# Kernel tuning notes

Hardware: AMD Instinct MI355X
Metric: run time of the kernel (lower is better)

## Reference

```python
import jax, jax.numpy as jnp
import numpy as np

B, T, D, E, H = 4, 2048, 1024, 4, 8
EPS = 1e-5


def _uniform(k, shape, bound):
    return jax.random.uniform(k, shape, jnp.float32, -bound, bound)


def setup_inputs() -> dict:
    key = jax.random.key(0)
    ks = jax.random.split(key, 12)
    wb = np.sqrt(6.0 / D) / np.sqrt(6.0)  # kaiming_uniform(a=sqrt5) bound ~ 1/sqrt(D)... keep simple
    wb = 1.0 / np.sqrt(D)
    return {
        "x": jax.random.normal(ks[0], (B, T, D), jnp.float32),
        "router_prob": jax.random.uniform(ks[1], (B, T, E), jnp.float32),
        "norm_w": jnp.ones((D,), jnp.float32),
        "norm_b": jnp.zeros((D,), jnp.float32),
        "q_w": _uniform(ks[2], (D, D), wb),
        "q_b": _uniform(ks[3], (D,), wb),
        "k_w": _uniform(ks[4], (D, D), wb),
        "k_b": _uniform(ks[5], (D,), wb),
        "v_w": _uniform(ks[6], (D, D), wb),
        "v_b": _uniform(ks[7], (D,), wb),
        "o_w": _uniform(ks[8], (D, D), wb),
        "o_b": _uniform(ks[9], (D,), wb),
    }


def _layernorm(x, w, b):
    mu = jnp.mean(x, axis=-1, keepdims=True)
    var = jnp.mean(jnp.square(x - mu), axis=-1, keepdims=True)
    return (x - mu) * jax.lax.rsqrt(var + EPS) * w + b


def reference(x, router_prob, norm_w, norm_b, q_w, q_b, k_w, k_b, v_w, v_b, o_w, o_b):
    e_cnt = router_prob.shape[2]
    b, t, d = x.shape
    n = t // e_cnt
    h = H
    scale = d ** (-0.5)  # note: original uses model_dim**-0.5, not head_dim

    qs, ks_, vs = [], [], []
    for e in range(e_cnt):
        xe = x[:, e * n:(e + 1) * n, :]
        xn = _layernorm(xe, norm_w, norm_b)
        m = d // (2 ** e)
        xm = xn[..., :m]  # [b, n, m] matryoshka slice
        # F.linear(xm, W[:, :m], bias): out = xm @ W[:, :m]^T + b -> [b, n, d]
        qs.append(jnp.einsum('bnm,dm->bnd', xm, q_w[:, :m]) + q_b)
        ks_.append(jnp.einsum('bnm,dm->bnd', xm, k_w[:, :m]) + k_b)
        vs.append(jnp.einsum('bnm,dm->bnd', xm, v_w[:, :m]) + v_b)
    q = jnp.concatenate(qs, axis=1)
    k = jnp.concatenate(ks_, axis=1)
    v = jnp.concatenate(vs, axis=1)

    dh = d // h
    q = q.reshape(b, t, h, dh).transpose(0, 2, 1, 3)  # b h t dh
    k = k.reshape(b, t, h, dh).transpose(0, 2, 1, 3)
    v = v.reshape(b, t, h, dh).transpose(0, 2, 1, 3)

    attn = jnp.einsum('bhqd,bhkd->bhqk', q, k) * scale
    attn = jax.nn.softmax(attn, axis=-1)  # dropout = identity in eval
    attn_out = jnp.einsum('bhqk,bhkd->bhqd', attn, v)
    attn_out = attn_out.transpose(0, 2, 1, 3).reshape(b, t, d)

    outs = []
    for e in range(e_cnt):
        sl = slice(e * n, (e + 1) * n)
        m = d // (2 ** e)
        xm = attn_out[:, sl, :m]
        out = jnp.einsum('bnm,om->bno', xm, o_w[:m, :m]) + o_b[:m]  # [b, n, m]
        pad = d - m
        if pad:
            out = jnp.pad(out, ((0, 0), (0, 0), (0, pad)))
        outs.append(out + x[:, sl, :])
    return jnp.concatenate(outs, axis=1)
```

## Files before the change

### kernel.cpp

```cpp
#include <hip/hip_runtime.h>
#include <hip/hip_bf16.h>

#define DEV static __device__ __forceinline__

typedef __attribute__((ext_vector_type(4))) float f32x4;
typedef __attribute__((ext_vector_type(8))) short s16x8;
typedef __attribute__((ext_vector_type(4))) unsigned int u32x4;

constexpr int Bn = 4, Tn = 2048, Dn = 1024, Hn = 8, DH = 128;
constexpr float EPSF = 1e-5f;
constexpr float QSCALE = 0.0450842200277801f;

DEV unsigned short f2bf(float f) {
    unsigned int u = __float_as_uint(f);
    u += 0x7FFF + ((u >> 16) & 1);
    return (unsigned short)(u >> 16);
}

DEV f32x4 mfma16(s16x8 a, s16x8 b, f32x4 c) {
    return __builtin_amdgcn_mfma_f32_16x16x32_bf16(a, b, c, 0, 0, 0);
}

DEV float ex2(float x) {
    float r;
    asm("v_exp_f32 %0, %1" : "=v"(r) : "v"(x));
    return r;
}

DEV unsigned int cvtpk(float lo, float hi) {
    unsigned int r;
    asm("v_cvt_pk_bf16_f32 %0, %1, %2" : "=v"(r) : "v"(lo), "v"(hi));
    return r;
}

typedef __attribute__((address_space(1))) const unsigned int GU32;
typedef __attribute__((address_space(3))) unsigned int LU32;
DEV void gload16(const void* g, void* l) {
    __builtin_amdgcn_global_load_lds((GU32*)g, (LU32*)l, 16, 0, 0);
}

__global__ __launch_bounds__(256) void cvtln_kernel(const float* __restrict__ x,
                                                    const float* __restrict__ w,
                                                    const float* __restrict__ b,
                                                    const float* __restrict__ qw,
                                                    const float* __restrict__ kw,
                                                    const float* __restrict__ vw,
                                                    const float* __restrict__ ow,
                                                    unsigned short* __restrict__ xn,
                                                    unsigned short* __restrict__ wb) {
    int bid = blockIdx.x;
    int tid = threadIdx.x;
    if (bid >= 8192) {
        int base = (bid - 8192) * 1024 + tid * 4;
        #pragma unroll
        for (int j = 0; j < 4; j++) {
            int idx = base + j;
            int sel = idx >> 20;
            int off = idx & (Dn * Dn - 1);
            const float* src = sel == 0 ? qw : sel == 1 ? kw : sel == 2 ? vw : ow;
            wb[idx] = f2bf(src[off]);
        }
        return;
    }
    int tok = bid;
    const float* xp = x + (size_t)tok * Dn;
    float4 v = ((const float4*)xp)[tid];
    float s = v.x + v.y + v.z + v.w;
    float q = v.x * v.x + v.y * v.y + v.z * v.z + v.w * v.w;
    for (int off = 32; off; off >>= 1) {
        s += __shfl_xor(s, off);
        q += __shfl_xor(q, off);
    }
    __shared__ float red[8];
    __shared__ float stats[2];
    int wid = tid >> 6, lane = tid & 63;
    if (lane == 0) { red[wid] = s; red[4 + wid] = q; }
    __syncthreads();
    if (tid == 0) {
        float ts = red[0] + red[1] + red[2] + red[3];
        float tq = red[4] + red[5] + red[6] + red[7];
        float mu = ts / Dn;
        float var = tq / Dn - mu * mu;
        stats[0] = mu;
        stats[1] = rsqrtf(var + EPSF);
    }
    __syncthreads();
    float mu = stats[0], rs = stats[1];
    int c = tid * 4;
    ushort4 o;
    o.x = f2bf((v.x - mu) * rs * w[c + 0] + b[c + 0]);
    o.y = f2bf((v.y - mu) * rs * w[c + 1] + b[c + 1]);
    o.z = f2bf((v.z - mu) * rs * w[c + 2] + b[c + 2]);
    o.w = f2bf((v.w - mu) * rs * w[c + 3] + b[c + 3]);
    ((ushort4*)(xn + (size_t)tok * Dn))[tid] = o;
}

__global__ __launch_bounds__(256) void qkv_gemm(const unsigned short* __restrict__ xn,
                                                const unsigned short* __restrict__ wmat,
                                                const float* __restrict__ qb_,
                                                const float* __restrict__ kb_,
                                                const float* __restrict__ vb_,
                                                unsigned short* __restrict__ outq,
                                                unsigned short* __restrict__ outk,
                                                unsigned short* __restrict__ vt) {
    int rowbase = blockIdx.x * 128;
    int colbase = blockIdx.y * 128;
    int matid = blockIdx.z;
    const unsigned short* W = wmat + (size_t)matid * Dn * Dn;
    const float* bias = matid == 0 ? qb_ : matid == 1 ? kb_ : vb_;
    float oscale = matid == 0 ? QSCALE : 1.0f;
    int e = (rowbase & (Tn - 1)) >> 9;
    int m = Dn >> e;
    int nt = m >> 5;

    __shared__ alignas(16) unsigned short At[3][128 * 32];
    __shared__ alignas(16) unsigned short Bt[3][128 * 32];

    int tid = threadIdx.x;
    int lane = tid & 63, wv = tid >> 6;
    int wr = (wv >> 1) * 64, wc = (wv & 1) * 64;
    int fr = lane & 15, fg = lane >> 4;
    int srow = tid >> 2, scol = (tid & 3) * 8;
    const unsigned short* ga0 = xn + (size_t)(rowbase + srow) * Dn + scol;
    const unsigned short* ga1 = xn + (size_t)(rowbase + 64 + srow) * Dn + scol;
    const unsigned short* gb0 = W + (size_t)(colbase + srow) * Dn + scol;
    const unsigned short* gb1 = W + (size_t)(colbase + 64 + srow) * Dn + scol;

    f32x4 acc[4][4] = {};

    auto STAGE = [&](int tt, int buf) {
        int kk = tt * 32;
        gload16(ga0 + kk, &At[buf][tid * 8]);
        gload16(ga1 + kk, &At[buf][2048 + tid * 8]);
        gload16(gb0 + kk, &Bt[buf][tid * 8]);
        gload16(gb1 + kk, &Bt[buf][2048 + tid * 8]);
    };

    STAGE(0, 0);
    if (nt > 1) STAGE(1, 1);

    int cur = 0, nxt2 = 2;
    for (int t = 0; t < nt; t++) {
        if (t + 1 < nt) { asm volatile("s_waitcnt vmcnt(4)" ::: "memory"); }
        else            { asm volatile("s_waitcnt vmcnt(0)" ::: "memory"); }
        __builtin_amdgcn_s_barrier();
        if (t + 2 < nt) STAGE(t + 2, nxt2);
        s16x8 a[4], b[4];
        #pragma unroll
        for (int i = 0; i < 4; i++) a[i] = *(const s16x8*)&At[cur][(wr + i * 16 + fr) * 32 + fg * 8];
        #pragma unroll
        for (int j = 0; j < 4; j++) b[j] = *(const s16x8*)&Bt[cur][(wc + j * 16 + fr) * 32 + fg * 8];
        #pragma unroll
        for (int i = 0; i < 4; i++)
            #pragma unroll
            for (int j = 0; j < 4; j++) acc[i][j] = mfma16(a[i], b[j], acc[i][j]);
        cur = cur == 2 ? 0 : cur + 1;
        nxt2 = nxt2 == 2 ? 0 : nxt2 + 1;
    }

    if (matid == 2) {
        #pragma unroll
        for (int i = 0; i < 4; i++)
            #pragma unroll
            for (int j = 0; j < 4; j++) {
                int col = colbase + wc + j * 16 + fr;
                float bv = bias[col];
                int row0 = rowbase + wr + i * 16 + fg * 4;
                int bb = row0 >> 11, tl = row0 & (Tn - 1);
                int w32 = tl & 31;
                int tlp = (tl & ~31) | (((w32 >> 2) & 3) * 8 + ((w32 >> 4) & 1) * 4);
                size_t base = (((size_t)bb * Hn + (col >> 7)) * DH + (col & (DH - 1))) * Tn + tlp;
                ushort4 o;
                o.x = f2bf(acc[i][j][0] + bv);
                o.y = f2bf(acc[i][j][1] + bv);
                o.z = f2bf(acc[i][j][2] + bv);
                o.w = f2bf(acc[i][j][3] + bv);
                *(ushort4*)&vt[base] = o;
            }
    } else {
        unsigned short* out = matid == 0 ? outq : outk;
        #pragma unroll
        for (int i = 0; i < 4; i++)
            #pragma unroll
            for (int j = 0; j < 4; j++) {
                int col = colbase + wc + j * 16 + fr;
                float bv = bias[col];
                #pragma unroll
                for (int r = 0; r < 4; r++) {
                    int row = rowbase + wr + i * 16 + fg * 4 + r;
                    out[(size_t)row * Dn + col] = f2bf((acc[i][j][r] + bv) * oscale);
                }
            }
    }
}

__global__ __launch_bounds__(512, 1) void attn_kernel(const unsigned short* __restrict__ Q,
                                                      const unsigned short* __restrict__ K,
                                                      const unsigned short* __restrict__ VT,
                                                      unsigned short* __restrict__ AO) {
    int f = blockIdx.x;
    int qi = f >> 5;
    int bh = f & 31;
    int b = bh >> 3, h = bh & 7;
    int qbase = qi * 256;
    int tid = threadIdx.x;
    int wv = tid >> 6, lane = tid & 63;
    int fr = lane & 15, fg = lane >> 4;

    __shared__ alignas(16) unsigned short Kt[2][128 * 128];
    __shared__ alignas(16) unsigned short Vt[2][128 * 128];

    s16x8 bq[2][4];
    #pragma unroll
    for (int hh = 0; hh < 2; hh++) {
        const size_t qr = ((size_t)b * Tn + qbase + wv * 32 + hh * 16 + fr) * Dn + h * DH;
        #pragma unroll
        for (int c = 0; c < 4; c++) bq[hh][c] = *(const s16x8*)&Q[qr + c * 32 + fg * 8];
    }

    const s16x8 ones = {(short)0x3F80, (short)0x3F80, (short)0x3F80, (short)0x3F80,
                        (short)0x3F80, (short)0x3F80, (short)0x3F80, (short)0x3F80};

    f32x4 acc[2][9] = {};
    float m_run[2] = {-1e30f, -1e30f};

    const unsigned short* Kbase = K + (size_t)b * Tn * Dn + h * DH;
    const unsigned short* Vbase = VT + ((size_t)b * Hn + h) * DH * Tn;

    int s_row_lo = tid >> 4, s_chk = tid & 15;

    auto STAGE = [&](int t, int buf) {
        int kb = t * 128;
        #pragma unroll
        for (int p = 0; p < 4; p++) {
            int row = p * 32 + s_row_lo;
            int chunk = s_chk ^ (row & 7);
            gload16(Kbase + (size_t)(kb + row) * Dn + chunk * 8,
                    &Kt[buf][p * 4096 + tid * 8]);
        }
        #pragma unroll
        for (int p = 0; p < 4; p++) {
            int row = p * 32 + s_row_lo;
            int chunk = s_chk ^ (row & 15);
            gload16(Vbase + (size_t)row * Tn + kb + chunk * 8,
                    &Vt[buf][p * 4096 + tid * 8]);
        }
    };

    STAGE(0, 0);
    __syncthreads();

    constexpr int NT = Tn / 128;
    for (int t = 0; t < NT; t++) {
        int cur = t & 1;
        if (t < NT - 1) STAGE(t + 1, cur ^ 1);

        const unsigned short* KtC = &Kt[cur][0];
        const unsigned short* VtC = &Vt[cur][0];

        f32x4 s[2][8] = {};
        __builtin_amdgcn_s_setprio(1);
        #pragma unroll
        for (int c = 0; c < 4; c++) {
            #pragma unroll
            for (int kt = 0; kt < 8; kt++) {
                s16x8 ak = *(const s16x8*)&KtC[(kt * 16 + fr) * 128 +
                                               (((c * 4 + fg) ^ (fr & 7)) * 8)];
                s[0][kt] = mfma16(ak, bq[0][c], s[0][kt]);
                s[1][kt] = mfma16(ak, bq[1][c], s[1][kt]);
            }
        }
        __builtin_amdgcn_s_setprio(0);

        float mx[2];
        #pragma unroll
        for (int hh = 0; hh < 2; hh++) {
            float v = s[hh][0][0];
            #pragma unroll
            for (int kt = 0; kt < 8; kt++)
                #pragma unroll
                for (int r = 0; r < 4; r++) v = fmaxf(v, s[hh][kt][r]);
            v = fmaxf(v, __shfl_xor(v, 16));
            v = fmaxf(v, __shfl_xor(v, 32));
            mx[hh] = v;
        }

        if (!__all(mx[0] - m_run[0] <= 8.0f && mx[1] - m_run[1] <= 8.0f)) {
            #pragma unroll
            for (int hh = 0; hh < 2; hh++) {
                float mnew = fmaxf(m_run[hh], mx[hh]);
                float fsc = ex2(m_run[hh] - mnew);
                float fw[4];
                #pragma unroll
                for (int r = 0; r < 4; r++) fw[r] = __shfl(fsc, fg * 4 + r);
                #pragma unroll
                for (int n = 0; n < 9; n++)
                    #pragma unroll
                    for (int r = 0; r < 4; r++) acc[hh][n][r] *= fw[r];
                m_run[hh] = mnew;
            }
        }

        s16x8 pa[2][4];
        #pragma unroll
        for (int hh = 0; hh < 2; hh++) {
            #pragma unroll
            for (int ks = 0; ks < 4; ks++) {
                float p0 = ex2(s[hh][ks * 2 + 0][0] - m_run[hh]);
                float p1 = ex2(s[hh][ks * 2 + 0][1] - m_run[hh]);
                float p2 = ex2(s[hh][ks * 2 + 0][2] - m_run[hh]);
                float p3 = ex2(s[hh][ks * 2 + 0][3] - m_run[hh]);
                float p4 = ex2(s[hh][ks * 2 + 1][0] - m_run[hh]);
                float p5 = ex2(s[hh][ks * 2 + 1][1] - m_run[hh]);
                float p6 = ex2(s[hh][ks * 2 + 1][2] - m_run[hh]);
                float p7 = ex2(s[hh][ks * 2 + 1][3] - m_run[hh]);
                u32x4 pw;
                pw.x = cvtpk(p0, p1);
                pw.y = cvtpk(p2, p3);
                pw.z = cvtpk(p4, p5);
                pw.w = cvtpk(p6, p7);
                pa[hh][ks] = __builtin_bit_cast(s16x8, pw);
            }
        }

        __builtin_amdgcn_s_setprio(1);
        #pragma unroll
        for (int ks = 0; ks < 4; ks++) {
            #pragma unroll
            for (int n = 0; n < 8; n++) {
                int row = n * 16 + fr;
                s16x8 bv = *(const s16x8*)&VtC[row * 128 +
                                               (((ks * 4 + fg) ^ (row & 15)) * 8)];
                acc[0][n] = mfma16(pa[0][ks], bv, acc[0][n]);
                acc[1][n] = mfma16(pa[1][ks], bv, acc[1][n]);
            }
            acc[0][8] = mfma16(pa[0][ks], ones, acc[0][8]);
            acc[1][8] = mfma16(pa[1][ks], ones, acc[1][8]);
        }
        __builtin_amdgcn_s_setprio(0);
        __syncthreads();
    }

    #pragma unroll
    for (int hh = 0; hh < 2; hh++) {
        float rl[4];
        #pragma unroll
        for (int r = 0; r < 4; r++) rl[r] = 1.0f / acc[hh][8][r];
        size_t orow0 = ((size_t)b * Tn + qbase + wv * 32 + hh * 16) * Dn + h * DH;
        for (int n = 0; n < 8; n++)
            for (int r = 0; r < 4; r++) {
                float v = acc[hh][n][r] * rl[r];
                AO[orow0 + (size_t)(fg * 4 + r) * Dn + n * 16 + fr] = f2bf(v);
            }
    }
}

__global__ __launch_bounds__(256) void oproj_gemm(const unsigned short* __restrict__ A,
                                                  const unsigned short* __restrict__ W,
                                                  const float* __restrict__ bias,
                                                  const float* __restrict__ x,
                                                  float* __restrict__ out) {
    int rowbase = blockIdx.x * 128;
    int colbase = blockIdx.y * 128;
    int e = (rowbase & (Tn - 1)) >> 9;
    int m = Dn >> e;
    int tid = threadIdx.x;

    if (colbase >= m) {
        #pragma unroll
        for (int i = 0; i < 16; i++) {
            int idx = i * 256 + tid;
            int r = idx >> 5, c4 = (idx & 31) * 4;
            size_t g = (size_t)(rowbase + r) * Dn + colbase + c4;
            *(float4*)&out[g] = *(const float4*)&x[g];
        }
        return;
    }

    __shared__ alignas(16) unsigned short At[3][128 * 32];
    __shared__ alignas(16) unsigned short Bt[3][128 * 32];
    int lane = tid & 63, wv = tid >> 6;
    int wr = (wv >> 1) * 64, wc = (wv & 1) * 64;
    int fr = lane & 15, fg = lane >> 4;
    int srow = tid >> 2, scol = (tid & 3) * 8;
    const unsigned short* ga0 = A + (size_t)(rowbase + srow) * Dn + scol;
    const unsigned short* ga1 = A + (size_t)(rowbase + 64 + srow) * Dn + scol;
    const unsigned short* gb0 = W + (size_t)(colbase + srow) * Dn + scol;
    const unsigned short* gb1 = W + (size_t)(colbase + 64 + srow) * Dn + scol;
    int nt = m >> 5;

    f32x4 acc[4][4] = {};

    auto STAGE = [&](int tt, int buf) {
        int kk = tt * 32;
        gload16(ga0 + kk, &At[buf][tid * 8]);
        gload16(ga1 + kk, &At[buf][2048 + tid * 8]);
        gload16(gb0 + kk, &Bt[buf][tid * 8]);
        gload16(gb1 + kk, &Bt[buf][2048 + tid * 8]);
    };

    STAGE(0, 0);
    if (nt > 1) STAGE(1, 1);

    int cur = 0, nxt2 = 2;
    for (int t = 0; t < nt; t++) {
        if (t + 1 < nt) { asm volatile("s_waitcnt vmcnt(4)" ::: "memory"); }
        else            { asm volatile("s_waitcnt vmcnt(0)" ::: "memory"); }
        __builtin_amdgcn_s_barrier();
        if (t + 2 < nt) STAGE(t + 2, nxt2);
        s16x8 a[4], b[4];
        #pragma unroll
        for (int i = 0; i < 4; i++) a[i] = *(const s16x8*)&At[cur][(wr + i * 16 + fr) * 32 + fg * 8];
        #pragma unroll
        for (int j = 0; j < 4; j++) b[j] = *(const s16x8*)&Bt[cur][(wc + j * 16 + fr) * 32 + fg * 8];
        #pragma unroll
        for (int i = 0; i < 4; i++)
            #pragma unroll
            for (int j = 0; j < 4; j++) acc[i][j] = mfma16(a[i], b[j], acc[i][j]);
        cur = cur == 2 ? 0 : cur + 1;
        nxt2 = nxt2 == 2 ? 0 : nxt2 + 1;
    }

    #pragma unroll
    for (int i = 0; i < 4; i++)
        #pragma unroll
        for (int j = 0; j < 4; j++) {
            int col = colbase + wc + j * 16 + fr;
            float bv = bias[col];
            #pragma unroll
            for (int r = 0; r < 4; r++) {
                int row = rowbase + wr + i * 16 + fg * 4 + r;
                size_t g = (size_t)row * Dn + col;
                out[g] = acc[i][j][r] + bv + x[g];
            }
        }
}

extern "C" void kernel_launch(void* const* d_in, const int* in_sizes, int n_in,
                              void* d_out, int out_size, void* d_ws, size_t ws_size,
                              hipStream_t stream) {
    const float* x   = (const float*)d_in[0];
    const float* nw  = (const float*)d_in[2];
    const float* nb  = (const float*)d_in[3];
    const float* qw  = (const float*)d_in[4];
    const float* qb_ = (const float*)d_in[5];
    const float* kw  = (const float*)d_in[6];
    const float* kb_ = (const float*)d_in[7];
    const float* vw  = (const float*)d_in[8];
    const float* vb_ = (const float*)d_in[9];
    const float* ow  = (const float*)d_in[10];
    const float* ob_ = (const float*)d_in[11];
    float* out = (float*)d_out;

    unsigned short* ws = (unsigned short*)d_ws;
    const size_t NTOK = (size_t)Bn * Tn;
    unsigned short* xn = ws;
    unsigned short* qd = xn + NTOK * Dn;
    unsigned short* kd = qd + NTOK * Dn;
    unsigned short* vt = kd + NTOK * Dn;
    unsigned short* ao = vt + NTOK * Dn;
    unsigned short* wb = ao + NTOK * Dn;

    hipLaunchKernelGGL(cvtln_kernel, dim3(12288), dim3(256), 0, stream,
                       x, nw, nb, qw, kw, vw, ow, xn, wb);
    hipLaunchKernelGGL(qkv_gemm, dim3(64, 8, 3), dim3(256), 0, stream,
                       xn, wb, qb_, kb_, vb_, qd, kd, vt);
    hipLaunchKernelGGL(attn_kernel, dim3(256), dim3(512), 0, stream, qd, kd, vt, ao);
    hipLaunchKernelGGL(oproj_gemm, dim3(64, 8), dim3(256), 0, stream,
                       ao, wb + (size_t)3 * Dn * Dn, ob_, x, out);
}
```

Baseline: 185.3 us.

## Shrink attention blocks and load V fragments directly from global memory

The attention kernel now uses 256-thread blocks covering 128 queries each, with twice as many blocks and two blocks per CU. The KV tile shrinks from 128 to 64 keys. V is no longer staged in LDS; each lane reads its MFMA B-fragments straight from the transposed V in global memory, and only K stays double-buffered in LDS. This is meant to cut LDS use and raise occupancy, at the cost of uncoalesced, L2-dependent V loads and twice as many loop iterations with barriers.

Measured after the change: 256.8 us. +38.6%, slower.

```diff
diff --git a/kernel.cpp b/kernel.cpp
--- a/kernel.cpp
+++ b/kernel.cpp
@@ -194,7 +194,7 @@
     }
 }
 
-__global__ __launch_bounds__(512, 1) void attn_kernel(const unsigned short* __restrict__ Q,
+__global__ __launch_bounds__(256, 2) void attn_kernel(const unsigned short* __restrict__ Q,
                                                       const unsigned short* __restrict__ K,
                                                       const unsigned short* __restrict__ VT,
                                                       unsigned short* __restrict__ AO) {
@@ -202,13 +202,12 @@
     int qi = f >> 5;
     int bh = f & 31;
     int b = bh >> 3, h = bh & 7;
-    int qbase = qi * 256;
+    int qbase = qi * 128;
     int tid = threadIdx.x;
     int wv = tid >> 6, lane = tid & 63;
     int fr = lane & 15, fg = lane >> 4;
 
-    __shared__ alignas(16) unsigned short Kt[2][128 * 128];
-    __shared__ alignas(16) unsigned short Vt[2][128 * 128];
+    __shared__ alignas(16) unsigned short Kt[2][64 * 128];
 
     s16x8 bq[2][4];
     #pragma unroll
@@ -226,44 +225,38 @@
 
     const unsigned short* Kbase = K + (size_t)b * Tn * Dn + h * DH;
     const unsigned short* Vbase = VT + ((size_t)b * Hn + h) * DH * Tn;
-
-    int s_row_lo = tid >> 4, s_chk = tid & 15;
+    const unsigned short* Vlane = Vbase + (size_t)fr * Tn + fg * 8;
+
+    int k_row_lo = tid >> 4, k_chk = tid & 15;
 
     auto STAGE = [&](int t, int buf) {
-        int kb = t * 128;
+        int kb = t * 64;
         #pragma unroll
         for (int p = 0; p < 4; p++) {
-            int row = p * 32 + s_row_lo;
-            int chunk = s_chk ^ (row & 7);
+            int row = p * 16 + k_row_lo;
+            int chunk = k_chk ^ (row & 7);
             gload16(Kbase + (size_t)(kb + row) * Dn + chunk * 8,
-                    &Kt[buf][p * 4096 + tid * 8]);
-        }
-        #pragma unroll
-        for (int p = 0; p < 4; p++) {
-            int row = p * 32 + s_row_lo;
-            int chunk = s_chk ^ (row & 15);
-            gload16(Vbase + (size_t)row * Tn + kb + chunk * 8,
-                    &Vt[buf][p * 4096 + tid * 8]);
+                    &Kt[buf][p * 2048 + tid * 8]);
         }
     };
 
     STAGE(0, 0);
     __syncthreads();
 
-    constexpr int NT = Tn / 128;
+    constexpr int NT = Tn / 64;
     for (int t = 0; t < NT; t++) {
         int cur = t & 1;
         if (t < NT - 1) STAGE(t + 1, cur ^ 1);
+        int kb = t * 64;
 
         const unsigned short* KtC = &Kt[cur][0];
-        const unsigned short* VtC = &Vt[cur][0];
-
-        f32x4 s[2][8] = {};
+
+        f32x4 s[2][4] = {};
         __builtin_amdgcn_s_setprio(1);
         #pragma unroll
         for (int c = 0; c < 4; c++) {
             #pragma unroll
-            for (int kt = 0; kt < 8; kt++) {
+            for (int kt = 0; kt < 4; kt++) {
                 s16x8 ak = *(const s16x8*)&KtC[(kt * 16 + fr) * 128 +
                                                (((c * 4 + fg) ^ (fr & 7)) * 8)];
                 s[0][kt] = mfma16(ak, bq[0][c], s[0][kt]);
@@ -272,12 +265,19 @@
         }
         __builtin_amdgcn_s_setprio(0);
 
+        s16x8 bv[2][8];
+        #pragma unroll
+        for (int ks = 0; ks < 2; ks++)
+            #pragma unroll
+            for (int n = 0; n < 8; n++)
+                bv[ks][n] = *(const s16x8*)(Vlane + (size_t)(n * 16) * Tn + kb + ks * 32);
+
         float mx[2];
         #pragma unroll
         for (int hh = 0; hh < 2; hh++) {
             float v = s[hh][0][0];
             #pragma unroll
-            for (int kt = 0; kt < 8; kt++)
+            for (int kt = 0; kt < 4; kt++)
                 #pragma unroll
                 for (int r = 0; r < 4; r++) v = fmaxf(v, s[hh][kt][r]);
             v = fmaxf(v, __shfl_xor(v, 16));
@@ -301,38 +301,32 @@
             }
         }
 
-        s16x8 pa[2][4];
+        s16x8 pa[2][2];
         #pragma unroll
         for (int hh = 0; hh < 2; hh++) {
-            #pragma unroll
-            for (int ks = 0; ks < 4; ks++) {
-                float p0 = ex2(s[hh][ks * 2 + 0][0] - m_run[hh]);
-                float p1 = ex2(s[hh][ks * 2 + 0][1] - m_run[hh]);
-                float p2 = ex2(s[hh][ks * 2 + 0][2] - m_run[hh]);
-                float p3 = ex2(s[hh][ks * 2 + 0][3] - m_run[hh]);
-                float p4 = ex2(s[hh][ks * 2 + 1][0] - m_run[hh]);
-                float p5 = ex2(s[hh][ks * 2 + 1][1] - m_run[hh]);
-                float p6 = ex2(s[hh][ks * 2 + 1][2] - m_run[hh]);
-                float p7 = ex2(s[hh][ks * 2 + 1][3] - m_run[hh]);
+            float p[16];
+            #pragma unroll
+            for (int kt = 0; kt < 4; kt++)
+                #pragma unroll
+                for (int r = 0; r < 4; r++) p[kt * 4 + r] = ex2(s[hh][kt][r] - m_run[hh]);
+            #pragma unroll
+            for (int ks = 0; ks < 2; ks++) {
                 u32x4 pw;
-                pw.x = cvtpk(p0, p1);
-                pw.y = cvtpk(p2, p3);
-                pw.z = cvtpk(p4, p5);
-                pw.w = cvtpk(p6, p7);
+                pw.x = cvtpk(p[ks * 8 + 0], p[ks * 8 + 1]);
+                pw.y = cvtpk(p[ks * 8 + 2], p[ks * 8 + 3]);
+                pw.z = cvtpk(p[ks * 8 + 4], p[ks * 8 + 5]);
+                pw.w = cvtpk(p[ks * 8 + 6], p[ks * 8 + 7]);
                 pa[hh][ks] = __builtin_bit_cast(s16x8, pw);
             }
         }
 
         __builtin_amdgcn_s_setprio(1);
         #pragma unroll
-        for (int ks = 0; ks < 4; ks++) {
+        for (int ks = 0; ks < 2; ks++) {
             #pragma unroll
             for (int n = 0; n < 8; n++) {
-                int row = n * 16 + fr;
-                s16x8 bv = *(const s16x8*)&VtC[row * 128 +
-                                               (((ks * 4 + fg) ^ (row & 15)) * 8)];
-                acc[0][n] = mfma16(pa[0][ks], bv, acc[0][n]);
-                acc[1][n] = mfma16(pa[1][ks], bv, acc[1][n]);
+                acc[0][n] = mfma16(pa[0][ks], bv[ks][n], acc[0][n]);
+                acc[1][n] = mfma16(pa[1][ks], bv[ks][n], acc[1][n]);
             }
             acc[0][8] = mfma16(pa[0][ks], ones, acc[0][8]);
             acc[1][8] = mfma16(pa[1][ks], ones, acc[1][8]);
@@ -465,7 +459,7 @@
                        x, nw, nb, qw, kw, vw, ow, xn, wb);
     hipLaunchKernelGGL(qkv_gemm, dim3(64, 8, 3), dim3(256), 0, stream,
                        xn, wb, qb_, kb_, vb_, qd, kd, vt);
-    hipLaunchKernelGGL(attn_kernel, dim3(256), dim3(512), 0, stream, qd, kd, vt, ao);
+    hipLaunchKernelGGL(attn_kernel, dim3(512), dim3(256), 0, stream, qd, kd, vt, ao);
     hipLaunchKernelGGL(oproj_gemm, dim3(64, 8), dim3(256), 0, stream,
                        ao, wb + (size_t)3 * Dn * Dn, ob_, x, out);
 }
```
